# Kernel optimization log

Measured on AMD Instinct MI355X. Metric: run time of the kernel, lower is better.

## Reference

```python
import jax, jax.numpy as jnp
import numpy as np

N = 100000      # nodes
E = 1600000     # edges
D_IN = 128
D_H = 128
D_OUT = 128


def setup_inputs() -> dict:
    key = jax.random.key(0)
    ks = jax.random.split(key, 8)
    x = jax.random.normal(ks[0], (N, D_IN), dtype=jnp.float32)
    edge_index = jax.random.randint(ks[1], (2, E), 0, N, dtype=jnp.int32)
    s = 1.0 / np.sqrt(D_IN)
    W1 = jax.random.uniform(ks[2], (D_IN, D_H), jnp.float32, -s, s)
    b1 = jnp.zeros((D_H,), jnp.float32)
    W2 = jax.random.uniform(ks[3], (D_H, D_H), jnp.float32, -s, s)
    b2 = jnp.zeros((D_H,), jnp.float32)
    W3 = jax.random.uniform(ks[4], (D_H, D_OUT), jnp.float32, -s, s)
    b3 = jnp.zeros((D_OUT,), jnp.float32)
    return {"x": x, "edge_index": edge_index,
            "W1": W1, "b1": b1, "W2": W2, "b2": b2, "W3": W3, "b3": b3}


def _gcn_conv(x, W, b, src, dst, norm, n_nodes):
    # PyG GCNConv: out = scatter_add(norm * (x @ W)[src] -> dst) + b
    h = x @ W
    msg = h[src] * norm[:, None]                       # [E+N, d]
    agg = jax.ops.segment_sum(msg, dst, num_segments=n_nodes)
    return agg + b


def reference(x, edge_index, W1, b1, W2, b2, W3, b3):
    n = x.shape[0]
    loop = jnp.arange(n, dtype=edge_index.dtype)
    src = jnp.concatenate([edge_index[0], loop])       # add self-loops
    dst = jnp.concatenate([edge_index[1], loop])
    # symmetric normalization: deg computed on target (incl. self-loops)
    deg = jax.ops.segment_sum(jnp.ones_like(dst, dtype=x.dtype), dst,
                              num_segments=n)
    dis = jnp.where(deg > 0, jax.lax.rsqrt(jnp.maximum(deg, 1.0)), 0.0)
    norm = dis[src] * dis[dst]                         # [E+N]

    h = _gcn_conv(x, W1, b1, src, dst, norm, n)
    h = jax.nn.relu(h)                                 # dropout: eval mode = identity
    h = _gcn_conv(h, W2, b2, src, dst, norm, n)
    h = jax.nn.relu(h)
    out = _gcn_conv(h, W3, b3, src, dst, norm, n)
    return out
```

## Files before the change

kernel.cpp:

```cpp
#include <hip/hip_runtime.h>
#include <hip/hip_fp16.h>

#define D 128
#define TPAD 136
#define NPB 256
#define KMAX 512
#define CHUNK 4096
#define SCAP 6144

typedef _Float16 half_t;
typedef _Float16 f16x8 __attribute__((ext_vector_type(8)));
typedef float f32x4 __attribute__((ext_vector_type(4)));


__global__ __launch_bounds__(256) void setup_kernel(const float* __restrict__ W1,
                                                    const float* __restrict__ W2,
                                                    const float* __restrict__ W3,
                                                    half_t* __restrict__ Wf1,
                                                    half_t* __restrict__ Wf2,
                                                    half_t* __restrict__ Wf3,
                                                    const int* __restrict__ dst,
                                                    int* __restrict__ bucket_cnt, int E) {
    __shared__ int scnt[KMAX];
    int b = blockIdx.x, t = threadIdx.x;
    if (b < 96) {
        const float* W = (b < 32) ? W1 : (b < 64) ? W2 : W3;
        half_t* Wf = (b < 32) ? Wf1 : (b < 64) ? Wf2 : Wf3;
        int bb = b & 31;
        int s = bb >> 3, tq = bb & 7;
        for (int e = t; e < 512; e += 256) {
            int l = e >> 3, j = e & 7;
            int k = s * 32 + ((l >> 4) & 3) * 4 + (j & 3) + ((j >> 2) << 4);
            int nn = tq * 16 + (l & 15);
            Wf[(size_t)((s * 8 + tq) * 64 + l) * 8 + j] = (half_t)W[k * 128 + nn];
        }
    } else if (b >= 98) {
        for (int i = t; i < KMAX; i += 256) scnt[i] = 0;
        __syncthreads();
        int base = (b - 98) * CHUNK;
        int nE = min(CHUNK, E - base);
        for (int i = t; i < nE; i += 256)
            atomicAdd(&scnt[dst[base + i] >> 8], 1);
        __syncthreads();
        for (int i = t; i < KMAX; i += 256)
            if (scnt[i]) atomicAdd(&bucket_cnt[i], scnt[i]);
    }
}

__global__ __launch_bounds__(KMAX) void bucket_scan_kernel(const int* __restrict__ bucket_cnt,
                                                           int* __restrict__ bucket_ptr,
                                                           int* __restrict__ bucket_cur,
                                                           int K, int E) {
    __shared__ int sh[KMAX];
    int t = threadIdx.x;
    int v = (t < K) ? bucket_cnt[t] : 0;
    sh[t] = v;
    __syncthreads();
    for (int off = 1; off < KMAX; off <<= 1) {
        int add = (t >= off) ? sh[t - off] : 0;
        __syncthreads();
        sh[t] += add;
        __syncthreads();
    }
    if (t < K) {
        int ex = sh[t] - v;
        bucket_ptr[t] = ex;
        bucket_cur[t] = ex;
    }
    if (t == 0) bucket_ptr[K] = E;
}

__global__ __launch_bounds__(256) void bucket_scatter_kernel(const int* __restrict__ src,
                                                             const int* __restrict__ dst,
                                                             int* __restrict__ bucket_cur,
                                                             int2* __restrict__ bdata, int E) {
    __shared__ int sdst[CHUNK];
    __shared__ int scnt[KMAX];
    __shared__ int sbase[KMAX];
    int t = threadIdx.x;
    int base = blockIdx.x * CHUNK;
    int nE = min(CHUNK, E - base);
    for (int i = t; i < KMAX; i += 256) scnt[i] = 0;
    __syncthreads();
    for (int i = t; i < nE; i += 256) {
        int d = dst[base + i];
        sdst[i] = d;
        atomicAdd(&scnt[d >> 8], 1);
    }
    __syncthreads();
    for (int i = t; i < KMAX; i += 256) {
        int c = scnt[i];
        sbase[i] = c ? atomicAdd(&bucket_cur[i], c) : 0;
        scnt[i] = 0;
    }
    __syncthreads();
    for (int i = t; i < nE; i += 256) {
        int d = sdst[i];
        int b = d >> 8;
        int pos = sbase[b] + atomicAdd(&scnt[b], 1);
        bdata[pos] = make_int2(src[base + i], d);
    }
}

__global__ __launch_bounds__(256) void csr_build_kernel(const int2* __restrict__ bdata,
                                                        const int* __restrict__ bucket_ptr,
                                                        int* __restrict__ row_ptr,
                                                        float* __restrict__ dis,
                                                        int* __restrict__ csr_src,
                                                        int n, int E, int K) {
    __shared__ int scnt[NPB];
    __shared__ int sh[NPB];
    __shared__ int2 sedge[SCAP];
    int b = blockIdx.x;
    int node0 = b << 8;
    int nn = min(NPB, n - node0);
    int t = threadIdx.x;
    int p0 = bucket_ptr[b], p1 = bucket_ptr[b + 1];
    int cnt = p1 - p0;
    bool stage = (cnt <= SCAP);
    scnt[t] = 0;
    __syncthreads();
    for (int i = t; i < cnt; i += 256) {
        int2 e = bdata[p0 + i];
        if (stage) sedge[i] = e;
        atomicAdd(&scnt[e.y - node0], 1);
    }
    __syncthreads();
    int v = scnt[t];
    sh[t] = v;
    __syncthreads();
    for (int off = 1; off < NPB; off <<= 1) {
        int add = (t >= off) ? sh[t - off] : 0;
        __syncthreads();
        sh[t] += add;
        __syncthreads();
    }
    int rowbase = p0 + sh[t] - v;
    if (t < nn) {
        row_ptr[node0 + t] = rowbase;
        dis[node0 + t] = rsqrtf((float)(v + 1));
    }
    if (b == K - 1 && t == 0) row_ptr[n] = E;
    scnt[t] = rowbase;
    __syncthreads();
    for (int i = t; i < cnt; i += 256) {
        int2 e = stage ? sedge[i] : bdata[p0 + i];
        int pos = atomicAdd(&scnt[e.y - node0], 1);
        csr_src[pos] = e.x;
    }
}


__device__ __forceinline__ void gemm_core_epilogue(half_t* sA, int tid, int base,
                                                   const float* __restrict__ dis,
                                                   half_t* __restrict__ C, int n,
                                                   f32x4 acc[8], int l, int w) {
    int m = l & 15, g = l >> 4;
    int R = w * 16;
    int row0 = base + R + 4 * g;
    float dd[4];
#pragma unroll
    for (int r = 0; r < 4; ++r) dd[r] = (row0 + r < n) ? dis[row0 + r] : 0.f;
    __syncthreads();
#pragma unroll
    for (int t = 0; t < 8; ++t) {
#pragma unroll
        for (int r = 0; r < 4; ++r)
            sA[(R + 4 * g + r) * TPAD + t * 16 + m] = (half_t)(acc[t][r] * dd[r]);
    }
    __syncthreads();
#pragma unroll
    for (int q = 0; q < 4; ++q) {
        int f4 = q * 256 + tid;
        int r = f4 >> 4, c = f4 & 15;
        int row = base + r;
        if (row < n)
            *(float4*)&C[(size_t)row * D + c * 8] = *(const float4*)&sA[r * TPAD + c * 8];
    }
}

__device__ __forceinline__ void gemm_mfma_loop(const half_t* sA, const half_t* __restrict__ Wf,
                                               f32x4 acc[8], int l, int w) {
    int m = l & 15, g = l >> 4;
    int R = w * 16;
    const f16x8* WF = (const f16x8*)Wf;
#pragma unroll
    for (int s = 0; s < 4; ++s) {
        union { f16x8 v; float2 f2[2]; } af;
        int a_off = (R + m) * TPAD + s * 32 + 4 * g;
        af.f2[0] = *(const float2*)&sA[a_off];
        af.f2[1] = *(const float2*)&sA[a_off + 16];
#pragma unroll
        for (int t = 0; t < 8; ++t) {
            f16x8 bf = WF[(size_t)(s * 8 + t) * 64 + l];
            acc[t] = __builtin_amdgcn_mfma_f32_16x16x32_f16(af.v, bf, acc[t], 0, 0, 0);
        }
    }
}

__global__ __launch_bounds__(256) void gemm_mfma_f32in(const float* __restrict__ A,
                                                       const half_t* __restrict__ Wf,
                                                       const float* __restrict__ dis,
                                                       half_t* __restrict__ C, int n) {
    __shared__ half_t sA[64 * TPAD];
    int tid = threadIdx.x;
    int base = blockIdx.x * 64;

    const float4* A4 = (const float4*)A;
#pragma unroll
    for (int it = 0; it < 8; ++it) {
        int idx = it * 256 + tid;
        int r = idx >> 5, kq = idx & 31;
        int grow = base + r;
        float4 va = (grow < n) ? A4[(size_t)grow * 32 + kq]
                               : make_float4(0.f, 0.f, 0.f, 0.f);
        union { half_t h[4]; float2 f2; } pk;
        pk.h[0] = (half_t)va.x; pk.h[1] = (half_t)va.y;
        pk.h[2] = (half_t)va.z; pk.h[3] = (half_t)va.w;
        *(float2*)&sA[r * TPAD + kq * 4] = pk.f2;
    }
    __syncthreads();

    int l = tid & 63, w = tid >> 6;
    f32x4 acc[8];
#pragma unroll
    for (int t = 0; t < 8; ++t) acc[t] = (f32x4){0.f, 0.f, 0.f, 0.f};
    gemm_mfma_loop(sA, Wf, acc, l, w);
    gemm_core_epilogue(sA, tid, base, dis, C, n, acc, l, w);
}

__global__ __launch_bounds__(256) void gemm_mfma_f16in(const half_t* __restrict__ A,
                                                       const half_t* __restrict__ Wf,
                                                       const float* __restrict__ dis,
                                                       half_t* __restrict__ C, int n) {
    __shared__ half_t sA[64 * TPAD];
    int tid = threadIdx.x;
    int base = blockIdx.x * 64;

    const float4* A4 = (const float4*)A;
#pragma unroll
    for (int it = 0; it < 4; ++it) {
        int idx = it * 256 + tid;
        int r = idx >> 4, c16 = idx & 15;
        int grow = base + r;
        float4 va = (grow < n) ? A4[(size_t)grow * 16 + c16]
                               : make_float4(0.f, 0.f, 0.f, 0.f);
        *(float4*)&sA[r * TPAD + c16 * 8] = va;
    }
    __syncthreads();

    int l = tid & 63, w = tid >> 6;
    f32x4 acc[8];
#pragma unroll
    for (int t = 0; t < 8; ++t) acc[t] = (f32x4){0.f, 0.f, 0.f, 0.f};
    gemm_mfma_loop(sA, Wf, acc, l, w);
    gemm_core_epilogue(sA, tid, base, dis, C, n, acc, l, w);
}


template <bool F16OUT>
__global__ __launch_bounds__(256) void aggregate_kernel(const __half2* __restrict__ Hs,
                                                        const int* __restrict__ row_ptr,
                                                        const int* __restrict__ csr_src,
                                                        const float* __restrict__ dis,
                                                        const float* __restrict__ b,
                                                        void* __restrict__ outv, int n) {
    int node = blockIdx.x * 4 + (threadIdx.x >> 6);
    if (node >= n) return;
    int lane = threadIdx.x & 63;

    float2 s0 = __half22float2(Hs[(size_t)node * 64 + lane]);
    float accx = s0.x, accy = s0.y;

    int p0 = row_ptr[node], p1 = row_ptr[node + 1];
    int p = p0;
    int nb8 = (p1 - p0) >> 3;
    if (nb8 > 0) {
        int idx[8];
#pragma unroll
        for (int u = 0; u < 8; ++u) idx[u] = csr_src[p + u];
        for (int bb = 1; bb < nb8; ++bb) {
            int nxt[8];
#pragma unroll
            for (int u = 0; u < 8; ++u) nxt[u] = csr_src[p + 8 + u];
            __half2 v[8];
#pragma unroll
            for (int u = 0; u < 8; ++u) v[u] = Hs[(size_t)idx[u] * 64 + lane];
#pragma unroll
            for (int u = 0; u < 8; ++u) {
                float2 f = __half22float2(v[u]);
                accx += f.x; accy += f.y;
            }
#pragma unroll
            for (int u = 0; u < 8; ++u) idx[u] = nxt[u];
            p += 8;
        }
        {
            __half2 v[8];
#pragma unroll
            for (int u = 0; u < 8; ++u) v[u] = Hs[(size_t)idx[u] * 64 + lane];
#pragma unroll
            for (int u = 0; u < 8; ++u) {
                float2 f = __half22float2(v[u]);
                accx += f.x; accy += f.y;
            }
            p += 8;
        }
    }
    for (; p + 4 <= p1; p += 4) {
        int s0i = csr_src[p + 0];
        int s1i = csr_src[p + 1];
        int s2i = csr_src[p + 2];
        int s3i = csr_src[p + 3];
        __half2 v0 = Hs[(size_t)s0i * 64 + lane];
        __half2 v1 = Hs[(size_t)s1i * 64 + lane];
        __half2 v2 = Hs[(size_t)s2i * 64 + lane];
        __half2 v3 = Hs[(size_t)s3i * 64 + lane];
        float2 f0 = __half22float2(v0), f1 = __half22float2(v1);
        float2 f2 = __half22float2(v2), f3 = __half22float2(v3);
        accx += f0.x; accy += f0.y;
        accx += f1.x; accy += f1.y;
        accx += f2.x; accy += f2.y;
        accx += f3.x; accy += f3.y;
    }
    for (; p < p1; ++p) {
        int s = csr_src[p];
        float2 f = __half22float2(Hs[(size_t)s * 64 + lane]);
        accx += f.x; accy += f.y;
    }

    float di = dis[node];
    float2 bb2 = *(const float2*)(b + 2 * lane);
    float ox = fmaf(accx, di, bb2.x);
    float oy = fmaf(accy, di, bb2.y);
    if (F16OUT) {
        ox = fmaxf(ox, 0.f);
        oy = fmaxf(oy, 0.f);
        ((__half2*)outv)[(size_t)node * 64 + lane] = __floats2half2_rn(ox, oy);
    } else {
        float2 o; o.x = ox; o.y = oy;
        ((float2*)((float*)outv + (size_t)node * D))[lane] = o;
    }
}


extern "C" void kernel_launch(void* const* d_in, const int* in_sizes, int n_in,
                              void* d_out, int out_size, void* d_ws, size_t ws_size,
                              hipStream_t stream) {
    const float* x  = (const float*)d_in[0];
    const int*   ei = (const int*)d_in[1];
    const float* W1 = (const float*)d_in[2];
    const float* b1 = (const float*)d_in[3];
    const float* W2 = (const float*)d_in[4];
    const float* b2 = (const float*)d_in[5];
    const float* W3 = (const float*)d_in[6];
    const float* b3 = (const float*)d_in[7];
    float* out = (float*)d_out;

    int n = in_sizes[0] / D;
    int E = in_sizes[1] / 2;
    const int* src = ei;
    const int* dst = ei + E;
    int K = (n + NPB - 1) >> 8;

    char* ws = (char*)d_ws;
    half_t* hbuf     = (half_t*)ws; ws += (size_t)n * D * sizeof(half_t);
    half_t* outh     = (half_t*)ws; ws += (size_t)n * D * sizeof(half_t);
    float* dis       = (float*)ws;  ws += (size_t)n * sizeof(float);
    int* row_ptr     = (int*)ws;    ws += (size_t)(n + 1) * sizeof(int);
    int* csr_src     = (int*)ws;    ws += (size_t)E * sizeof(int);
    int* bucket_cnt  = (int*)ws;    ws += KMAX * sizeof(int);
    int* bucket_ptr  = (int*)ws;    ws += (KMAX + 1) * sizeof(int);
    int* bucket_cur  = (int*)ws;    ws += KMAX * sizeof(int);
    ws = (char*)(((uintptr_t)ws + 15) & ~(uintptr_t)15);
    half_t* Wf1      = (half_t*)ws; ws += 128 * 128 * sizeof(half_t);
    half_t* Wf2      = (half_t*)ws; ws += 128 * 128 * sizeof(half_t);
    half_t* Wf3      = (half_t*)ws; ws += 128 * 128 * sizeof(half_t);
    int2* bdata      = (int2*)hbuf;

    int gC = (E + CHUNK - 1) / CHUNK;
    int gM = (n + 63) / 64;
    int gA = (n + 3) / 4;

    hipMemsetAsync(bucket_cnt, 0, KMAX * sizeof(int), stream);
    setup_kernel<<<98 + gC, 256, 0, stream>>>(W1, W2, W3, Wf1, Wf2, Wf3,
                                              dst, bucket_cnt, E);
    bucket_scan_kernel<<<1, KMAX, 0, stream>>>(bucket_cnt, bucket_ptr, bucket_cur, K, E);
    bucket_scatter_kernel<<<gC, 256, 0, stream>>>(src, dst, bucket_cur, bdata, E);
    csr_build_kernel<<<K, 256, 0, stream>>>(bdata, bucket_ptr, row_ptr, dis, csr_src, n, E, K);

    gemm_mfma_f32in<<<gM, 256, 0, stream>>>(x, Wf1, dis, hbuf, n);
    aggregate_kernel<true><<<gA, 256, 0, stream>>>((const __half2*)hbuf, row_ptr, csr_src, dis, b1, outh, n);
    gemm_mfma_f16in<<<gM, 256, 0, stream>>>(outh, Wf2, dis, hbuf, n);
    aggregate_kernel<true><<<gA, 256, 0, stream>>>((const __half2*)hbuf, row_ptr, csr_src, dis, b2, outh, n);
    gemm_mfma_f16in<<<gM, 256, 0, stream>>>(outh, Wf3, dis, hbuf, n);
    aggregate_kernel<false><<<gA, 256, 0, stream>>>((const __half2*)hbuf, row_ptr, csr_src, dis, b3, out, n);
}
```

Baseline: 416.2 us.

## Pack bucketed edges into 32-bit words and double GEMM rows per block

Bucketed edges are stored as one 32-bit word holding a 17-bit source id and the 8-bit local destination, instead of an int2. This halves the traffic of the bucket scatter and CSR build passes and the LDS staging size. Separately, each GEMM block now handles 128 rows with two accumulator sets, so each weight fragment loaded is reused across two MFMAs and the grid has half as many blocks. The packing assumes node ids fit in 17 bits (n ≤ 131072), and the GEMM change raises register and LDS use per block.

```diff
diff --git a/kernel.cpp b/kernel.cpp
--- a/kernel.cpp
+++ b/kernel.cpp
@@ -7,6 +7,7 @@
 #define KMAX 512
 #define CHUNK 4096
 #define SCAP 6144
+#define SRCMASK 0x1FFFF
 
 typedef _Float16 half_t;
 typedef _Float16 f16x8 __attribute__((ext_vector_type(8)));
@@ -73,7 +74,7 @@
 __global__ __launch_bounds__(256) void bucket_scatter_kernel(const int* __restrict__ src,
                                                              const int* __restrict__ dst,
                                                              int* __restrict__ bucket_cur,
-                                                             int2* __restrict__ bdata, int E) {
+                                                             int* __restrict__ bpack, int E) {
     __shared__ int sdst[CHUNK];
     __shared__ int scnt[KMAX];
     __shared__ int sbase[KMAX];
@@ -98,11 +99,11 @@
         int d = sdst[i];
         int b = d >> 8;
         int pos = sbase[b] + atomicAdd(&scnt[b], 1);
-        bdata[pos] = make_int2(src[base + i], d);
-    }
-}
-
-__global__ __launch_bounds__(256) void csr_build_kernel(const int2* __restrict__ bdata,
+        bpack[pos] = src[base + i] | ((d & 255) << 17);
+    }
+}
+
+__global__ __launch_bounds__(256) void csr_build_kernel(const int* __restrict__ bpack,
                                                         const int* __restrict__ bucket_ptr,
                                                         int* __restrict__ row_ptr,
                                                         float* __restrict__ dis,
@@ -110,7 +111,7 @@
                                                         int n, int E, int K) {
     __shared__ int scnt[NPB];
     __shared__ int sh[NPB];
-    __shared__ int2 sedge[SCAP];
+    __shared__ int sedge[SCAP];
     int b = blockIdx.x;
     int node0 = b << 8;
     int nn = min(NPB, n - node0);
@@ -121,9 +122,9 @@
     scnt[t] = 0;
     __syncthreads();
     for (int i = t; i < cnt; i += 256) {
-        int2 e = bdata[p0 + i];
+        int e = bpack[p0 + i];
         if (stage) sedge[i] = e;
-        atomicAdd(&scnt[e.y - node0], 1);
+        atomicAdd(&scnt[(e >> 17) & 255], 1);
     }
     __syncthreads();
     int v = scnt[t];
@@ -144,33 +145,62 @@
     scnt[t] = rowbase;
     __syncthreads();
     for (int i = t; i < cnt; i += 256) {
-        int2 e = stage ? sedge[i] : bdata[p0 + i];
-        int pos = atomicAdd(&scnt[e.y - node0], 1);
-        csr_src[pos] = e.x;
-    }
-}
-
-
-__device__ __forceinline__ void gemm_core_epilogue(half_t* sA, int tid, int base,
-                                                   const float* __restrict__ dis,
-                                                   half_t* __restrict__ C, int n,
-                                                   f32x4 acc[8], int l, int w) {
+        int e = stage ? sedge[i] : bpack[p0 + i];
+        int pos = atomicAdd(&scnt[(e >> 17) & 255], 1);
+        csr_src[pos] = e & SRCMASK;
+    }
+}
+
+
+__device__ __forceinline__ void gemm_mfma_loop2(const half_t* sA, const half_t* __restrict__ Wf,
+                                                f32x4 acc0[8], f32x4 acc1[8], int l, int w) {
     int m = l & 15, g = l >> 4;
     int R = w * 16;
-    int row0 = base + R + 4 * g;
-    float dd[4];
-#pragma unroll
-    for (int r = 0; r < 4; ++r) dd[r] = (row0 + r < n) ? dis[row0 + r] : 0.f;
+    const f16x8* WF = (const f16x8*)Wf;
+#pragma unroll
+    for (int s = 0; s < 4; ++s) {
+        union { f16x8 v; float2 f2[2]; } a0, a1;
+        int off0 = (R + m) * TPAD + s * 32 + 4 * g;
+        int off1 = off0 + 64 * TPAD;
+        a0.f2[0] = *(const float2*)&sA[off0];
+        a0.f2[1] = *(const float2*)&sA[off0 + 16];
+        a1.f2[0] = *(const float2*)&sA[off1];
+        a1.f2[1] = *(const float2*)&sA[off1 + 16];
+#pragma unroll
+        for (int t = 0; t < 8; ++t) {
+            f16x8 bf = WF[(size_t)(s * 8 + t) * 64 + l];
+            acc0[t] = __builtin_amdgcn_mfma_f32_16x16x32_f16(a0.v, bf, acc0[t], 0, 0, 0);
+            acc1[t] = __builtin_amdgcn_mfma_f32_16x16x32_f16(a1.v, bf, acc1[t], 0, 0, 0);
+        }
+    }
+}
+
+__device__ __forceinline__ void gemm_epilogue2(half_t* sA, int tid, int base,
+                                               const float* __restrict__ dis,
+                                               half_t* __restrict__ C, int n,
+                                               f32x4 acc0[8], f32x4 acc1[8], int l, int w) {
+    int m = l & 15, g = l >> 4;
+    int R = w * 16;
+    int r0 = base + R + 4 * g;
+    int r1 = r0 + 64;
+    float dd0[4], dd1[4];
+#pragma unroll
+    for (int r = 0; r < 4; ++r) {
+        dd0[r] = (r0 + r < n) ? dis[r0 + r] : 0.f;
+        dd1[r] = (r1 + r < n) ? dis[r1 + r] : 0.f;
+    }
     __syncthreads();
 #pragma unroll
     for (int t = 0; t < 8; ++t) {
 #pragma unroll
-        for (int r = 0; r < 4; ++r)
-            sA[(R + 4 * g + r) * TPAD + t * 16 + m] = (half_t)(acc[t][r] * dd[r]);
-    }
-    __syncthreads();
-#pragma unroll
-    for (int q = 0; q < 4; ++q) {
+        for (int r = 0; r < 4; ++r) {
+            sA[(R + 4 * g + r) * TPAD + t * 16 + m] = (half_t)(acc0[t][r] * dd0[r]);
+            sA[(64 + R + 4 * g + r) * TPAD + t * 16 + m] = (half_t)(acc1[t][r] * dd1[r]);
+        }
+    }
+    __syncthreads();
+#pragma unroll
+    for (int q = 0; q < 8; ++q) {
         int f4 = q * 256 + tid;
         int r = f4 >> 4, c = f4 & 15;
         int row = base + r;
@@ -179,36 +209,17 @@
     }
 }
 
-__device__ __forceinline__ void gemm_mfma_loop(const half_t* sA, const half_t* __restrict__ Wf,
-                                               f32x4 acc[8], int l, int w) {
-    int m = l & 15, g = l >> 4;
-    int R = w * 16;
-    const f16x8* WF = (const f16x8*)Wf;
-#pragma unroll
-    for (int s = 0; s < 4; ++s) {
-        union { f16x8 v; float2 f2[2]; } af;
-        int a_off = (R + m) * TPAD + s * 32 + 4 * g;
-        af.f2[0] = *(const float2*)&sA[a_off];
-        af.f2[1] = *(const float2*)&sA[a_off + 16];
-#pragma unroll
-        for (int t = 0; t < 8; ++t) {
-            f16x8 bf = WF[(size_t)(s * 8 + t) * 64 + l];
-            acc[t] = __builtin_amdgcn_mfma_f32_16x16x32_f16(af.v, bf, acc[t], 0, 0, 0);
-        }
-    }
-}
-
 __global__ __launch_bounds__(256) void gemm_mfma_f32in(const float* __restrict__ A,
                                                        const half_t* __restrict__ Wf,
                                                        const float* __restrict__ dis,
                                                        half_t* __restrict__ C, int n) {
-    __shared__ half_t sA[64 * TPAD];
+    __shared__ half_t sA[128 * TPAD];
     int tid = threadIdx.x;
-    int base = blockIdx.x * 64;
+    int base = blockIdx.x * 128;
 
     const float4* A4 = (const float4*)A;
 #pragma unroll
-    for (int it = 0; it < 8; ++it) {
+    for (int it = 0; it < 16; ++it) {
         int idx = it * 256 + tid;
         int r = idx >> 5, kq = idx & 31;
         int grow = base + r;
@@ -222,24 +233,27 @@
     __syncthreads();
 
     int l = tid & 63, w = tid >> 6;
-    f32x4 acc[8];
-#pragma unroll
-    for (int t = 0; t < 8; ++t) acc[t] = (f32x4){0.f, 0.f, 0.f, 0.f};
-    gemm_mfma_loop(sA, Wf, acc, l, w);
-    gemm_core_epilogue(sA, tid, base, dis, C, n, acc, l, w);
+    f32x4 acc0[8], acc1[8];
+#pragma unroll
+    for (int t = 0; t < 8; ++t) {
+        acc0[t] = (f32x4){0.f, 0.f, 0.f, 0.f};
+        acc1[t] = (f32x4){0.f, 0.f, 0.f, 0.f};
+    }
+    gemm_mfma_loop2(sA, Wf, acc0, acc1, l, w);
+    gemm_epilogue2(sA, tid, base, dis, C, n, acc0, acc1, l, w);
 }
 
 __global__ __launch_bounds__(256) void gemm_mfma_f16in(const half_t* __restrict__ A,
                                                        const half_t* __restrict__ Wf,
                                                        const float* __restrict__ dis,
                                                        half_t* __restrict__ C, int n) {
-    __shared__ half_t sA[64 * TPAD];
+    __shared__ half_t sA[128 * TPAD];
     int tid = threadIdx.x;
-    int base = blockIdx.x * 64;
+    int base = blockIdx.x * 128;
 
     const float4* A4 = (const float4*)A;
 #pragma unroll
-    for (int it = 0; it < 4; ++it) {
+    for (int it = 0; it < 8; ++it) {
         int idx = it * 256 + tid;
         int r = idx >> 4, c16 = idx & 15;
         int grow = base + r;
@@ -250,11 +264,14 @@
     __syncthreads();
 
     int l = tid & 63, w = tid >> 6;
-    f32x4 acc[8];
-#pragma unroll
-    for (int t = 0; t < 8; ++t) acc[t] = (f32x4){0.f, 0.f, 0.f, 0.f};
-    gemm_mfma_loop(sA, Wf, acc, l, w);
-    gemm_core_epilogue(sA, tid, base, dis, C, n, acc, l, w);
+    f32x4 acc0[8], acc1[8];
+#pragma unroll
+    for (int t = 0; t < 8; ++t) {
+        acc0[t] = (f32x4){0.f, 0.f, 0.f, 0.f};
+        acc1[t] = (f32x4){0.f, 0.f, 0.f, 0.f};
+    }
+    gemm_mfma_loop2(sA, Wf, acc0, acc1, l, w);
+    gemm_epilogue2(sA, tid, base, dis, C, n, acc0, acc1, l, w);
 }
 
 
@@ -376,18 +393,18 @@
     half_t* Wf1      = (half_t*)ws; ws += 128 * 128 * sizeof(half_t);
     half_t* Wf2      = (half_t*)ws; ws += 128 * 128 * sizeof(half_t);
     half_t* Wf3      = (half_t*)ws; ws += 128 * 128 * sizeof(half_t);
-    int2* bdata      = (int2*)hbuf;
+    int* bpack       = (int*)hbuf;
 
     int gC = (E + CHUNK - 1) / CHUNK;
-    int gM = (n + 63) / 64;
+    int gM = (n + 127) / 128;
     int gA = (n + 3) / 4;
 
     hipMemsetAsync(bucket_cnt, 0, KMAX * sizeof(int), stream);
     setup_kernel<<<98 + gC, 256, 0, stream>>>(W1, W2, W3, Wf1, Wf2, Wf3,
                                               dst, bucket_cnt, E);
     bucket_scan_kernel<<<1, KMAX, 0, stream>>>(bucket_cnt, bucket_ptr, bucket_cur, K, E);
-    bucket_scatter_kernel<<<gC, 256, 0, stream>>>(src, dst, bucket_cur, bdata, E);
-    csr_build_kernel<<<K, 256, 0, stream>>>(bdata, bucket_ptr, row_ptr, dis, csr_src, n, E, K);
+    bucket_scatter_kernel<<<gC, 256, 0, stream>>>(src, dst, bucket_cur, bpack, E);
+    csr_build_kernel<<<K, 256, 0, stream>>>(bpack, bucket_ptr, row_ptr, dis, csr_src, n, E, K);
 
     gemm_mfma_f32in<<<gM, 256, 0, stream>>>(x, Wf1, dis, hbuf, n);
     aggregate_kernel<true><<<gA, 256, 0, stream>>>((const __half2*)hbuf, row_ptr, csr_src, dis, b1, outh, n);
```

New measurement: 438.7 us. 5.4% more time.
